# Performance work log

Hardware: AMD Instinct MI355X
Metric: run time of the kernel (lower is better)

## Reference

```python
import jax, jax.numpy as jnp
import numpy as np

EPS = 1e-7
R = 3  # routing iterations


def conv(x, k, b, stride):
    y = jax.lax.conv_general_dilated(x, k, (stride, stride), 'VALID',
                                     dimension_numbers=('NHWC', 'HWIO', 'NHWC'))
    return y + b


def squash(s):
    n = jnp.linalg.norm(s, axis=-1, keepdims=True)
    return (n * n) / (1.0 + n * n) * s / (n + EPS)


def setup_inputs() -> dict:
    key = jax.random.key(0)
    ks = jax.random.split(key, 12)
    B = 256

    def g(k, shape, scale=0.05):
        return jax.random.normal(k, shape, dtype=jnp.float32) * scale

    return dict(
        x=jax.random.normal(ks[0], (B, 40, 40, 1), dtype=jnp.float32),
        y=jax.random.randint(ks[1], (B,), 0, 10),
        conv1_k=g(ks[2], (5, 5, 1, 64)),   conv1_b=jnp.zeros((64,), jnp.float32),
        conv2_k=g(ks[3], (9, 9, 64, 128)), conv2_b=jnp.zeros((128,), jnp.float32),
        conv3_k=g(ks[4], (9, 9, 128, 256)), conv3_b=jnp.zeros((256,), jnp.float32),
        prim_k=g(ks[5], (9, 9, 256, 256)), prim_b=jnp.zeros((256,), jnp.float32),
        w=g(ks[6], (1152, 10, 16, 8)),
        d1_w=g(ks[7], (160, 1024)),  d1_b=jnp.zeros((1024,), jnp.float32),
        d2_w=g(ks[8], (1024, 2048)), d2_b=jnp.zeros((2048,), jnp.float32),
        d3_w=g(ks[9], (2048, 1600)), d3_b=jnp.zeros((1600,), jnp.float32),
    )


def reference(x, y, conv1_k, conv1_b, conv2_k, conv2_b, conv3_k, conv3_b,
              prim_k, prim_b, w, d1_w, d1_b, d2_w, d2_b, d3_w, d3_b):
    # conv stack: 40 -> 36 -> 28 -> 20 -> 6 (primary caps, stride 2, linear)
    h = jax.nn.relu(conv(x, conv1_k, conv1_b, 1))
    h = jax.nn.relu(conv(h, conv2_k, conv2_b, 1))
    h = jax.nn.relu(conv(h, conv3_k, conv3_b, 1))
    h = conv(h, prim_k, prim_b, 2)                      # [B,6,6,256]
    B = h.shape[0]
    u = h.reshape(B, 1152, 8)                           # 1152 primary capsules of dim 8

    # pose predictions: u_hat[b,i,j,k] = sum_v w[i,j,k,v] * u[b,i,v]
    u_hat = jnp.einsum('ijkv,biv->bijk', w, u)          # [B,1152,10,16]

    # dynamic routing by agreement
    b_logit = jnp.zeros((B, 1152, 10), dtype=u_hat.dtype)
    for _ in range(R):
        c = jax.nn.softmax(b_logit, axis=2)[..., None]          # [B,1152,10,1]
        s = jnp.sum(c * u_hat, axis=1, keepdims=True)           # [B,1,10,16]
        v = squash(s)                                           # [B,1,10,16]
        b_logit = b_logit + jnp.sum(u_hat * v, axis=-1)         # agreement

    # masking by true label and reconstruction
    yh = jax.nn.one_hot(y, 10, dtype=v.dtype)                   # [B,10]
    v_masked = yh[:, None, :, None] * v                         # [B,1,10,16]
    v_flat = v_masked.reshape(B, 10 * 16)
    r1 = jax.nn.relu(v_flat @ d1_w + d1_b)
    r2 = jax.nn.relu(r1 @ d2_w + d2_b)
    recon = jax.nn.sigmoid(r2 @ d3_w + d3_b)                    # [B,1600]
    return (v, recon)
```

## Files before the change

kernel.cpp:

```cpp
#include <hip/hip_runtime.h>
#include <hip/hip_bf16.h>

typedef _Float16 f16;
typedef __attribute__((ext_vector_type(8))) _Float16 f16x8;
typedef __attribute__((ext_vector_type(4))) float f32x4;

__device__ __forceinline__ void gload_lds16(const void* g, void* l) {
  __builtin_amdgcn_global_load_lds((const __attribute__((address_space(1))) void*)g,
                                   (__attribute__((address_space(3))) void*)l, 16, 0, 0);
}

__device__ __forceinline__ void wtrans_body(const float* __restrict__ src,
                                            f16* __restrict__ dst,
                                            int K, int N, int k0, int n0) {
  __shared__ float tile[64][65];
  int t = threadIdx.x;
#pragma unroll
  for (int i = 0; i < 16; ++i) {
    int id = t + i * 256;
    int r = id >> 6, c = id & 63;
    tile[r][c] = (n0 + c < N) ? src[(size_t)(k0 + r) * N + n0 + c] : 0.f;
  }
  __syncthreads();
#pragma unroll
  for (int i = 0; i < 16; ++i) {
    int id = t + i * 256;
    int r = id >> 6, c = id & 63;
    dst[(size_t)(n0 + r) * K + k0 + c] = (f16)tile[c][r];
  }
}

__global__ __launch_bounds__(256) void wprepc_kernel(const float* __restrict__ s0, f16* __restrict__ d0,
                                                     const float* __restrict__ s1, f16* __restrict__ d1,
                                                     const float* __restrict__ s2, f16* __restrict__ d2,
                                                     const float* __restrict__ x,
                                                     const float* __restrict__ c1k,
                                                     const float* __restrict__ c1b,
                                                     f16* __restrict__ h1) {
  int bid = (int)blockIdx.x;
  if (bid < 162) {
    int bx = bid % 81, by = bid / 81;
    wtrans_body(s0, d0, 5184, 128, bx * 64, by * 64);
  } else if (bid < 810) {
    int l = bid - 162; int bx = l % 162, by = l / 162;
    wtrans_body(s1, d1, 10368, 256, bx * 64, by * 64);
  } else if (bid < 2106) {
    int l = bid - 810; int bx = l % 324, by = l / 324;
    wtrans_body(s2, d2, 20736, 256, bx * 64, by * 64);
  } else {
    int idx = (bid - 2106) * 256 + threadIdx.x;
    int g = idx & 7;
    int co0 = g * 8;
    int r = idx >> 3;
    int ow = r % 36; int r2 = r / 36; int oh = r2 % 36; int b = r2 / 36;
    float acc[8];
#pragma unroll
    for (int j = 0; j < 8; ++j) acc[j] = c1b[co0 + j];
    const float* xp = x + (b * 40 + oh) * 40 + ow;
#pragma unroll
    for (int dy = 0; dy < 5; ++dy)
#pragma unroll
      for (int dx = 0; dx < 5; ++dx) {
        float xv = xp[dy * 40 + dx];
        const float* kp = c1k + (dy * 5 + dx) * 64 + co0;
#pragma unroll
        for (int j = 0; j < 8; ++j) acc[j] += xv * kp[j];
      }
    f16x8 o;
#pragma unroll
    for (int j = 0; j < 8; ++j) o[j] = (f16)fmaxf(acc[j], 0.f);
    *(f16x8*)(h1 + r * 64 + co0) = o;
  }
}

__global__ __launch_bounds__(256) void wprepd_kernel(const float* __restrict__ s0, f16* __restrict__ d0,
                                                     const float* __restrict__ s1, f16* __restrict__ d1) {
  int bid = (int)blockIdx.x;
  if (bid < 512) {
    int bx = bid % 16, by = bid / 16;
    wtrans_body(s0, d0, 1024, 2048, bx * 64, by * 64);
  } else {
    int l = bid - 512; int bx = l % 32, by = l / 32;
    wtrans_body(s1, d1, 2048, 1600, bx * 64, by * 64);
  }
}

template<int CIN, int WIN>
__device__ __forceinline__ int tapA_off(int kt) {
  int tap, ci0;
  if (CIN == 64)       { tap = kt;      ci0 = 0; }
  else if (CIN == 128) { tap = kt >> 1; ci0 = (kt & 1) << 6; }
  else                 { tap = kt >> 2; ci0 = (kt & 3) << 6; }
  int dy = tap / 9, dx = tap - dy * 9;
  return (dy * WIN + dx) * CIN + ci0;
}

template<int HIN, int WIN, int CIN, int HOUT, int WOUT, int COUT, int STRIDE,
         bool RELU, bool OUTF16, int FULLB, int TAILB>
__global__ __launch_bounds__(512, 2) void conv8p_kernel(const f16* __restrict__ in,
                                                        const f16* __restrict__ wt,
                                                        const float* __restrict__ bias,
                                                        f16* __restrict__ out16,
                                                        float* __restrict__ out32,
                                                        f16* __restrict__ tp01,
                                                        f16* __restrict__ tp2) {
  static_assert(COUT == 256, "BN=256 template requires COUT==256");
  constexpr int KTOT = 81 * CIN;
  constexpr int NT = KTOT / 64;
  static_assert(TAILB == 0 || NT % 3 == 0, "K-third split requires NT%3==0");
  constexpr int PNT = (TAILB > 0) ? NT / 3 : NT;
  __shared__ __align__(16) f16 lds[65536];
  const int bid = (int)blockIdx.x;
  int mb, kt0, kt1;
  f16* tp = nullptr;
  if (TAILB == 0 || bid < FULLB) {
    mb = bid; kt0 = 0; kt1 = NT;
  } else {
    int idx = bid - FULLB;
    int piece = idx / TAILB;
    int loc = idx - piece * TAILB;
    mb = FULLB + loc;
    kt0 = piece * PNT; kt1 = kt0 + PNT;
    tp = (piece < 2 ? tp01 + (size_t)piece * TAILB * 65536 : tp2) + (size_t)loc * 65536;
  }
  const int t = threadIdx.x;
  const int wave = t >> 6, lane = t & 63;
  const int hi = lane >> 4, lo = lane & 15;
  const int wm = wave >> 2, wn = wave & 3;

  int Aoff[4], Boff[4];
  {
    int g = (lane & 7) ^ ((lane >> 3) & 7);
#pragma unroll
    for (int rbi = 0; rbi < 4; ++rbi) {
      int r = rbi * 64 + 8 * wave + (lane >> 3);
      int m = mb * 256 + r;
      int b = m / (HOUT * WOUT);
      int rr = m - b * (HOUT * WOUT);
      int oh = rr / WOUT, ow = rr - oh * WOUT;
      Aoff[rbi] = ((b * HIN + oh * STRIDE) * WIN + ow * STRIDE) * CIN + g * 8;
      Boff[rbi] = r * KTOT + g * 8;
    }
  }
  const int gb0 = (hi ^ (lo & 7)) << 4;
  const int gb1 = ((4 + hi) ^ (lo & 7)) << 4;

  const char* ldsc = (const char*)lds;
  char* ldsw = (char*)lds;

#define GA(rbi, tpo, bq) gload_lds16(in + Aoff[rbi] + (tpo),                        \
    (void*)(ldsw + (bq) * 32768 + ((rbi) * 64 + 8 * wave) * 128))
#define GB(rbi, tile) gload_lds16(wt + Boff[rbi] + ((tile) << 6),                   \
    (void*)(ldsw + 65536 + ((tile) & 1) * 32768 + ((rbi) * 64 + 8 * wave) * 128))

  {
    int tq = tapA_off<CIN, WIN>(kt0);
    int bq = kt0 & 1;
    GA(0, tq, bq); GA(2, tq, bq); GA(1, tq, bq); GA(3, tq, bq);
    GB(0, kt0); GB(1, kt0); GB(2, kt0); GB(3, kt0);
    GB(0, kt0 + 1); GB(1, kt0 + 1); GB(2, kt0 + 1); GB(3, kt0 + 1);
    asm volatile("s_waitcnt vmcnt(4)" ::: "memory");
    __builtin_amdgcn_s_barrier();
  }

  f32x4 acc[8][4] = {};

#define DO_PHASE(Q, STAGE)                                                          \
  {                                                                                 \
    f16x8 af[2][2];                                                                 \
    _Pragma("unroll")                                                               \
    for (int mf = 0; mf < 2; ++mf) {                                                \
      af[mf][0] = *(const f16x8*)(Ab + ((Q) * 2 + mf) * 2048 + gb0);                \
      af[mf][1] = *(const f16x8*)(Ab + ((Q) * 2 + mf) * 2048 + gb1);                \
    }                                                                               \
    STAGE;                                                                          \
    __builtin_amdgcn_s_barrier();                                                   \
    asm volatile("s_waitcnt lgkmcnt(0)" ::: "memory");                              \
    __builtin_amdgcn_sched_barrier(0);                                              \
    __builtin_amdgcn_s_setprio(1);                                                  \
    _Pragma("unroll")                                                               \
    for (int sb = 0; sb < 2; ++sb)                                                  \
      _Pragma("unroll")                                                             \
      for (int mf = 0; mf < 2; ++mf)                                                \
        _Pragma("unroll")                                                           \
        for (int nf = 0; nf < 4; ++nf)                                              \
          acc[(Q) * 2 + mf][nf] = __builtin_amdgcn_mfma_f32_16x16x32_f16(           \
              af[mf][sb], bfr[nf][sb], acc[(Q) * 2 + mf][nf], 0, 0, 0);             \
    __builtin_amdgcn_s_setprio(0);                                                  \
    __builtin_amdgcn_s_barrier();                                                   \
  }

  for (int T = kt0; T < kt1; ++T) {
    const int q = T & 1;
    const char* Ab = ldsc + q * 32768 + wm * 16384 + lo * 128;
    const char* Bb = ldsc + 65536 + q * 32768 + wn * 8192 + lo * 128;
    const int tpn = tapA_off<CIN, WIN>(T + 1);
    f16x8 bfr[4][2];
#pragma unroll
    for (int nf = 0; nf < 4; ++nf) {
      bfr[nf][0] = *(const f16x8*)(Bb + nf * 2048 + gb0);
      bfr[nf][1] = *(const f16x8*)(Bb + nf * 2048 + gb1);
    }
    DO_PHASE(0, if (T + 1 < kt1) { GA(0, tpn, (T + 1) & 1); GA(2, tpn, (T + 1) & 1); })
    DO_PHASE(1, if (T + 1 < kt1) { GA(1, tpn, (T + 1) & 1); GA(3, tpn, (T + 1) & 1); })
    DO_PHASE(2, if (T + 2 < kt1) { GB(0, T + 2); GB(1, T + 2); })
    DO_PHASE(3,
      if (T + 2 < kt1) {
        GB(2, T + 2); GB(3, T + 2);
        asm volatile("s_waitcnt vmcnt(4)" ::: "memory");
      } else {
        asm volatile("s_waitcnt vmcnt(0)" ::: "memory");
      })
  }
#undef DO_PHASE
#undef GA
#undef GB

  if (tp == nullptr) {
#pragma unroll
    for (int mfr = 0; mfr < 8; ++mfr) {
#pragma unroll
      for (int nf = 0; nf < 4; ++nf) {
        int m0 = mb * 256 + wm * 128 + mfr * 16 + hi * 4;
        int n = wn * 64 + nf * 16 + lo;
        float bval = bias[n];
#pragma unroll
        for (int r = 0; r < 4; ++r) {
          float v = acc[mfr][nf][r] + bval;
          if (RELU) v = fmaxf(v, 0.f);
          int o = (m0 + r) * COUT + n;
          if (OUTF16) out16[o] = (f16)v; else out32[o] = v;
        }
      }
    }
  } else {
#pragma unroll
    for (int mfr = 0; mfr < 8; ++mfr) {
#pragma unroll
      for (int nf = 0; nf < 4; ++nf) {
        int rowloc = wm * 128 + mfr * 16 + hi * 4;
        int n = wn * 64 + nf * 16 + lo;
#pragma unroll
        for (int r = 0; r < 4; ++r)
          tp[(rowloc + r) * 256 + n] = (f16)acc[mfr][nf][r];
      }
    }
  }
}

__global__ __launch_bounds__(256) void tailred3_kernel(const f16* __restrict__ tp01,
                                                       const f16* __restrict__ tp2,
                                                       const float* __restrict__ bias,
                                                       f16* __restrict__ h3) {
  int idx = blockIdx.x * 256 + threadIdx.x;
  int e0 = idx * 8;
  int n0 = e0 & 255;
  f16x8 a = *(const f16x8*)(tp01 + e0);
  f16x8 b = *(const f16x8*)(tp01 + 9437184 + e0);
  f16x8 c = *(const f16x8*)(tp2 + e0);
  f16x8 o;
#pragma unroll
  for (int j = 0; j < 8; ++j) {
    float v = (float)a[j] + (float)b[j] + (float)c[j] + bias[n0 + j];
    o[j] = (f16)fmaxf(v, 0.f);
  }
  *(f16x8*)(h3 + 16777216 + e0) = o;
}

template<int HIN, int WIN, int CIN, int HOUT, int WOUT, int COUT, int STRIDE,
         bool RELU, bool OUTF16, int SPLIT, bool ADDBIAS>
__global__ __launch_bounds__(256) void conv_mfma_kernel(const f16* __restrict__ in,
                                                        const f16* __restrict__ wt,
                                                        const float* __restrict__ bias,
                                                        f16* __restrict__ out16,
                                                        float* __restrict__ out32) {
  constexpr int KTOT = 81 * CIN;
  constexpr int NBLK = COUT / 128;
  constexpr int MTOT = 256 * HOUT * WOUT;
  constexpr int MBNB = (MTOT / 128) * NBLK;
  constexpr int NKT = (KTOT / 64) / SPLIT;
  __shared__ __align__(16) f16 lds[16384];
  int bidx = (int)blockIdx.x;
  int ks = 0;
  if (SPLIT > 1) { ks = bidx / MBNB; bidx -= ks * MBNB; }
  const int mb = bidx / NBLK;
  const int nb = bidx % NBLK;
  const int t = threadIdx.x;
  const int wave = t >> 6, lane = t & 63;
  const int hi = lane >> 4, lo = lane & 15;
  const bool isA = wave < 2;
  const int slot0 = wave << 9;

  int baseoff[8];
#pragma unroll
  for (int it = 0; it < 8; ++it) {
    int s = slot0 + it * 64 + lane;
    if (isA) {
      int row = s >> 3;
      int g = (s & 7) ^ (row & 7);
      int mg = mb * 128 + row;
      int b = mg / (HOUT * WOUT);
      int rr = mg - b * (HOUT * WOUT);
      int oh = rr / WOUT;
      int ow = rr - oh * WOUT;
      baseoff[it] = ((b * HIN + oh * STRIDE) * WIN + ow * STRIDE) * CIN + g * 8;
    } else {
      int sl = s - 1024;
      int row = sl >> 3;
      int g = (sl & 7) ^ (row & 7);
      baseoff[it] = (nb * 128 + row) * KTOT + g * 8;
    }
  }
  const f16* gsrc = isA ? in : wt;

  int aQ[4], bQ[4];
  const int wm = wave >> 1, wn = wave & 1;
#pragma unroll
  for (int f = 0; f < 4; ++f) {
    int arow = wm * 64 + f * 16 + lo;
    aQ[f] = (arow * 128) ^ ((arow & 7) << 4);
    int brow = wn * 64 + f * 16 + lo;
    bQ[f] = 16384 + ((brow * 128) ^ ((brow & 7) << 4));
  }

  f32x4 acc[4][4] = {};
  const char* ldsc = (const char*)lds;

  const int kt0 = ks * NKT;
  for (int kt = kt0; kt < kt0 + NKT; ++kt) {
    int tapoff;
    if (isA) tapoff = tapA_off<CIN, WIN>(kt);
    else     tapoff = kt << 6;
    __syncthreads();
#pragma unroll
    for (int it = 0; it < 8; ++it)
      gload_lds16(gsrc + baseoff[it] + tapoff,
                  (void*)((char*)lds + ((slot0 + it * 64) << 4)));
    __syncthreads();
#pragma unroll
    for (int sub = 0; sub < 2; ++sub) {
      const int gx = (sub * 4 + hi) << 4;
      f16x8 av[4], bv[4];
#pragma unroll
      for (int f = 0; f < 4; ++f) av[f] = *(const f16x8*)(ldsc + (aQ[f] ^ gx));
#pragma unroll
      for (int f = 0; f < 4; ++f) bv[f] = *(const f16x8*)(ldsc + (bQ[f] ^ gx));
#pragma unroll
      for (int mf = 0; mf < 4; ++mf)
#pragma unroll
        for (int nf = 0; nf < 4; ++nf)
          acc[mf][nf] = __builtin_amdgcn_mfma_f32_16x16x32_f16(av[mf], bv[nf],
                                                               acc[mf][nf], 0, 0, 0);
    }
  }

  float* o32 = out32 + (size_t)ks * MTOT * COUT;
#pragma unroll
  for (int mf = 0; mf < 4; ++mf) {
#pragma unroll
    for (int nf = 0; nf < 4; ++nf) {
      int m0 = mb * 128 + wm * 64 + mf * 16 + hi * 4;
      int n = nb * 128 + wn * 64 + nf * 16 + lo;
      float bval = ADDBIAS ? bias[n] : 0.f;
#pragma unroll
      for (int r = 0; r < 4; ++r) {
        float v = acc[mf][nf][r] + bval;
        if (RELU) v = fmaxf(v, 0.f);
        int o = (m0 + r) * COUT + n;
        if (OUTF16) out16[o] = (f16)v; else o32[o] = v;
      }
    }
  }
}

template<int K, int NP, int SPLIT>
__global__ __launch_bounds__(256) void gemm_mfma_kernel(const f16* __restrict__ A,
                                                        const f16* __restrict__ Bw,
                                                        float* __restrict__ dpart) {
  constexpr int NBLK = NP / 128;
  constexpr int MBNB = 2 * NBLK;
  constexpr int NKT = (K / 64) / SPLIT;
  __shared__ __align__(16) f16 lds[16384];
  int bidx = (int)blockIdx.x;
  int ks = 0;
  if (SPLIT > 1) { ks = bidx / MBNB; bidx -= ks * MBNB; }
  const int mb = bidx / NBLK;
  const int nb = bidx % NBLK;
  const int t = threadIdx.x;
  const int wave = t >> 6, lane = t & 63;
  const int hi = lane >> 4, lo = lane & 15;
  const bool isA = wave < 2;
  const int slot0 = wave << 9;

  int baseoff[8];
#pragma unroll
  for (int it = 0; it < 8; ++it) {
    int s = slot0 + it * 64 + lane;
    if (isA) {
      int row = s >> 3;
      int g = (s & 7) ^ (row & 7);
      baseoff[it] = (mb * 128 + row) * K + g * 8;
    } else {
      int sl = s - 1024;
      int row = sl >> 3;
      int g = (sl & 7) ^ (row & 7);
      baseoff[it] = (nb * 128 + row) * K + g * 8;
    }
  }
  const f16* gsrc = isA ? A : Bw;

  int aQ[4], bQ[4];
  const int wm = wave >> 1, wn = wave & 1;
#pragma unroll
  for (int f = 0; f < 4; ++f) {
    int arow = wm * 64 + f * 16 + lo;
    aQ[f] = (arow * 128) ^ ((arow & 7) << 4);
    int brow = wn * 64 + f * 16 + lo;
    bQ[f] = 16384 + ((brow * 128) ^ ((brow & 7) << 4));
  }

  f32x4 acc[4][4] = {};
  const char* ldsc = (const char*)lds;

  const int kt0 = ks * NKT;
  for (int kt = kt0; kt < kt0 + NKT; ++kt) {
    int tapoff = kt << 6;
    __syncthreads();
#pragma unroll
    for (int it = 0; it < 8; ++it)
      gload_lds16(gsrc + baseoff[it] + tapoff,
                  (void*)((char*)lds + ((slot0 + it * 64) << 4)));
    __syncthreads();
#pragma unroll
    for (int sub = 0; sub < 2; ++sub) {
      const int gx = (sub * 4 + hi) << 4;
      f16x8 av[4], bv[4];
#pragma unroll
      for (int f = 0; f < 4; ++f) av[f] = *(const f16x8*)(ldsc + (aQ[f] ^ gx));
#pragma unroll
      for (int f = 0; f < 4; ++f) bv[f] = *(const f16x8*)(ldsc + (bQ[f] ^ gx));
#pragma unroll
      for (int mf = 0; mf < 4; ++mf)
#pragma unroll
        for (int nf = 0; nf < 4; ++nf)
          acc[mf][nf] = __builtin_amdgcn_mfma_f32_16x16x32_f16(av[mf], bv[nf],
                                                               acc[mf][nf], 0, 0, 0);
    }
  }

  float* o32 = dpart + (size_t)ks * 256 * NP;
#pragma unroll
  for (int mf = 0; mf < 4; ++mf) {
#pragma unroll
    for (int nf = 0; nf < 4; ++nf) {
      int m0 = mb * 128 + wm * 64 + mf * 16 + hi * 4;
      int n = nb * 128 + wn * 64 + nf * 16 + lo;
#pragma unroll
      for (int r = 0; r < 4; ++r)
        o32[(m0 + r) * NP + n] = acc[mf][nf][r];
    }
  }
}

__global__ __launch_bounds__(256) void d2red_kernel(const float* __restrict__ part,
                                                    const float* __restrict__ bias,
                                                    f16* __restrict__ r2) {
  int idx = blockIdx.x * 256 + threadIdx.x;
  int e0 = idx * 4;
  int n0 = e0 & 2047;
  float4 a = *(const float4*)(part + e0);
  const float4 b1 = *(const float4*)(part + 524288 + e0);
  const float4 b2 = *(const float4*)(part + 1048576 + e0);
  const float4 b3 = *(const float4*)(part + 1572864 + e0);
  float v[4] = {a.x + b1.x + b2.x + b3.x, a.y + b1.y + b2.y + b3.y,
                a.z + b1.z + b2.z + b3.z, a.w + b1.w + b2.w + b3.w};
#pragma unroll
  for (int j = 0; j < 4; ++j)
    r2[e0 + j] = (f16)fmaxf(v[j] + bias[n0 + j], 0.f);
}

__global__ __launch_bounds__(256) void d3red_kernel(const float* __restrict__ part,
                                                    const float* __restrict__ bias,
                                                    float* __restrict__ recon) {
  int idx = blockIdx.x * 256 + threadIdx.x;
  int e0 = idx * 4;
  int n0 = e0 % 1664;
  int m = e0 / 1664;
  float v[4] = {0.f, 0.f, 0.f, 0.f};
#pragma unroll
  for (int s = 0; s < 8; ++s) {
    float4 a = *(const float4*)(part + s * 425984 + e0);
    v[0] += a.x; v[1] += a.y; v[2] += a.z; v[3] += a.w;
  }
#pragma unroll
  for (int j = 0; j < 4; ++j) {
    int n = n0 + j;
    if (n < 1600)
      recon[m * 1600 + n] = 1.f / (1.f + expf(-(v[j] + bias[n])));
  }
}

__global__ __launch_bounds__(320) void uhatps_kernel(const float* __restrict__ wf,
                                                     const float* __restrict__ part,
                                                     const float* __restrict__ pbias,
                                                     f16* __restrict__ uh,
                                                     float* __restrict__ parts) {
  __shared__ float pl[8][128][8];
  int blk = (int)blockIdx.x;
  int ic = blk / 32, bg = blk - ic * 32;
  int b0 = bg * 8;
  int t = threadIdx.x;
  for (int e = t; e < 8192; e += 320) {
    int b8 = e >> 10;
    int el = e & 1023;
    float a = pbias[el & 255];
    int gi = (b0 + b8) * 9216 + ic * 1024 + el;
#pragma unroll
    for (int s = 0; s < 6; ++s) a += part[s * 2359296 + gi];
    pl[b8][el >> 3][el & 7] = a;
  }
  __syncthreads();
  int half = (t >= 160) ? 1 : 0;
  int jk = t - half * 160;
  int ibase = ic * 128 + half * 64;
  float sum[8] = {};
  for (int il = 0; il < 64; ++il) {
    int i = ibase + il;
    const float4* w4 = (const float4*)(wf + (i * 160 + jk) * 8);
    float4 w0 = w4[0], w1 = w4[1];
    int row = half * 64 + il;
#pragma unroll
    for (int b8 = 0; b8 < 8; ++b8) {
      const float* pr = pl[b8][row];
      float acc = w0.x * pr[0] + w0.y * pr[1] + w0.z * pr[2] + w0.w * pr[3] +
                  w1.x * pr[4] + w1.y * pr[5] + w1.z * pr[6] + w1.w * pr[7];
      uh[((size_t)(b0 + b8) * 1152 + i) * 160 + jk] = (f16)acc;
      sum[b8] += acc;
    }
  }
#pragma unroll
  for (int b8 = 0; b8 < 8; ++b8)
    parts[((b0 + b8) * 18 + ic * 2 + half) * 160 + jk] = sum[b8];
}

template<int NCH, bool FIRST, bool WRITEB>
__global__ __launch_bounds__(256) void ba_kernel(const f16* __restrict__ uh,
                                                 const float* __restrict__ psrc,
                                                 float cscale,
                                                 float* __restrict__ blog,
                                                 float* __restrict__ pdst) {
  __shared__ f16 ul[128 * 172];
  __shared__ float vl[160];
  __shared__ float csm[128 * 10];
  int blk = (int)blockIdx.x;
  int b = blk / 9, ic = blk - b * 9;
  int t = threadIdx.x;
  const f16* ub = uh + (size_t)(b * 1152 + ic * 128) * 160;
  for (int e = t; e < 2560; e += 256) {
    int row = e / 20, col = e - row * 20;
    *(f16x8*)(ul + row * 172 + col * 8) = *(const f16x8*)(ub + row * 160 + col * 8);
  }
  if (t < 160) {
    float s = 0.f;
    for (int c = 0; c < NCH; ++c) s += psrc[(b * NCH + c) * 160 + t];
    s *= cscale;
    float ss = s * s;
    ss += __shfl_xor(ss, 1, 16);
    ss += __shfl_xor(ss, 2, 16);
    ss += __shfl_xor(ss, 4, 16);
    ss += __shfl_xor(ss, 8, 16);
    float n = sqrtf(ss);
    float f = ss / ((1.f + ss) * (n + 1e-7f));
    vl[t] = f * s;
  }
  __syncthreads();

  int il = t >> 1, half = t & 1, j0 = half * 5;
  const f16* ur = ul + il * 172 + j0 * 16;
  float agr[5];
#pragma unroll
  for (int j = 0; j < 5; ++j) {
    f16x8 a0 = *(const f16x8*)(ur + j * 16);
    f16x8 a1 = *(const f16x8*)(ur + j * 16 + 8);
    const float* vv = vl + (j0 + j) * 16;
    float s = (float)a0[0] * vv[0] + (float)a0[1] * vv[1] + (float)a0[2] * vv[2] +
              (float)a0[3] * vv[3] + (float)a0[4] * vv[4] + (float)a0[5] * vv[5] +
              (float)a0[6] * vv[6] + (float)a0[7] * vv[7] +
              (float)a1[0] * vv[8] + (float)a1[1] * vv[9] + (float)a1[2] * vv[10] +
              (float)a1[3] * vv[11] + (float)a1[4] * vv[12] + (float)a1[5] * vv[13] +
              (float)a1[6] * vv[14] + (float)a1[7] * vv[15];
    agr[j] = s;
  }
  int bbase = (b * 1152 + ic * 128 + il) * 10 + j0;
  float bl[5];
#pragma unroll
  for (int j = 0; j < 5; ++j) bl[j] = (FIRST ? 0.f : blog[bbase + j]) + agr[j];
  if (WRITEB) {
#pragma unroll
    for (int j = 0; j < 5; ++j) blog[bbase + j] = bl[j];
  }
  float mx = bl[0];
#pragma unroll
  for (int j = 1; j < 5; ++j) mx = fmaxf(mx, bl[j]);
  mx = fmaxf(mx, __shfl_xor(mx, 1));
  float e5[5], se = 0.f;
#pragma unroll
  for (int j = 0; j < 5; ++j) { e5[j] = expf(bl[j] - mx); se += e5[j]; }
  se += __shfl_xor(se, 1);
  float inv = 1.f / se;
#pragma unroll
  for (int j = 0; j < 5; ++j) csm[il * 10 + j0 + j] = e5[j] * inv;
  __syncthreads();

  if (t < 160) {
    int j = t >> 4;
    float s = 0.f;
    for (int il2 = 0; il2 < 128; ++il2)
      s += csm[il2 * 10 + j] * (float)ul[il2 * 172 + t];
    pdst[(b * 9 + ic) * 160 + t] = s;
  }
}

__global__ __launch_bounds__(1024) void maskd1v_kernel(const float* __restrict__ parts,
                                                       const int* __restrict__ y,
                                                       const float* __restrict__ w1,
                                                       const float* __restrict__ b1,
                                                       float* __restrict__ vout,
                                                       f16* __restrict__ r1) {
  __shared__ float vl[160];
  int b = blockIdx.x, t = threadIdx.x;
  if (t < 160) {
    float s = 0.f;
    for (int c = 0; c < 9; ++c) s += parts[(b * 9 + c) * 160 + t];
    float ss = s * s;
    ss += __shfl_xor(ss, 1, 16);
    ss += __shfl_xor(ss, 2, 16);
    ss += __shfl_xor(ss, 4, 16);
    ss += __shfl_xor(ss, 8, 16);
    float n = sqrtf(ss);
    float f = ss / ((1.f + ss) * (n + 1e-7f));
    float v = f * s;
    vl[t] = v;
    vout[b * 160 + t] = v;
  }
  __syncthreads();
  int yb = y[b];
  float acc = b1[t];
#pragma unroll
  for (int k = 0; k < 16; ++k) acc += vl[yb * 16 + k] * w1[(yb * 16 + k) * 1024 + t];
  r1[b * 1024 + t] = (f16)fmaxf(acc, 0.f);
}

extern "C" void kernel_launch(void* const* d_in, const int* in_sizes, int n_in,
                              void* d_out, int out_size, void* d_ws, size_t ws_size,
                              hipStream_t stream) {
  const float* x       = (const float*)d_in[0];
  const int*   y       = (const int*)d_in[1];
  const float* conv1_k = (const float*)d_in[2];
  const float* conv1_b = (const float*)d_in[3];
  const float* conv2_k = (const float*)d_in[4];
  const float* conv2_b = (const float*)d_in[5];
  const float* conv3_k = (const float*)d_in[6];
  const float* conv3_b = (const float*)d_in[7];
  const float* prim_k  = (const float*)d_in[8];
  const float* prim_b  = (const float*)d_in[9];
  const float* w_route = (const float*)d_in[10];
  const float* d1_w = (const float*)d_in[11];
  const float* d1_b = (const float*)d_in[12];
  const float* d2_w = (const float*)d_in[13];
  const float* d2_b = (const float*)d_in[14];
  const float* d3_w = (const float*)d_in[15];
  const float* d3_b = (const float*)d_in[16];

  char* ws = (char*)d_ws;
  f16*   h1      = (f16*)(ws + 0);
  f16*   tpart01 = (f16*)(ws + 0);
  float* part    = (float*)(ws + 0);
  float* dpart2  = (float*)(ws + 0);
  float* dpart3  = (float*)(ws + 16777216);
  f16*   h2      = (f16*)(ws + 42467328);
  f16*   uhat    = (f16*)(ws + 56623104);
  f16*   h3      = (f16*)(ws + 93847552);
  f16*   tpart2  = (f16*)(ws + 146276352);
  float* parts_a = (float*)(ws + 150994944);
  float* parts_b = (float*)(ws + 153944064);
  float* blog    = (float*)(ws + 155713536);
  f16*   r1h     = (f16*)(ws + 167673856);
  f16*   r2h     = (f16*)(ws + 168198144);
  f16*   wt2     = (f16*)(ws + 170819584);
  f16*   wt3     = (f16*)(ws + 172146688);
  f16*   wtp     = (f16*)(ws + 177455104);
  f16*   wd2     = (f16*)(ws + 177455104);
  f16*   wd3     = (f16*)(ws + 181649408);

  float* vout  = (float*)d_out;
  float* recon = (float*)d_out + 40960;

  wprepc_kernel<<<12474, 256, 0, stream>>>(conv2_k, wt2, conv3_k, wt3, prim_k, wtp,
                                           x, conv1_k, conv1_b, h1);

  conv_mfma_kernel<36, 36, 64, 28, 28, 128, 1, true, true, 1, true>
      <<<1568, 256, 0, stream>>>(h1, wt2, conv2_b, h2, nullptr);
  conv8p_kernel<28, 28, 128, 20, 20, 256, 1, true, true, 256, 144>
      <<<688, 512, 0, stream>>>(h2, wt3, conv3_b, h3, nullptr, tpart01, tpart2);
  tailred3_kernel<<<4608, 256, 0, stream>>>(tpart01, tpart2, conv3_b, h3);
  conv_mfma_kernel<20, 20, 256, 6, 6, 256, 2, false, false, 6, false>
      <<<864, 256, 0, stream>>>(h3, wtp, prim_b, nullptr, part);

  uhatps_kernel<<<288, 320, 0, stream>>>(w_route, part, prim_b, uhat, parts_a);
  wprepd_kernel<<<1344, 256, 0, stream>>>(d2_w, wd2, d3_w, wd3);
  ba_kernel<18, true, true><<<2304, 256, 0, stream>>>(uhat, parts_a, 0.1f, blog, parts_b);
  ba_kernel<9, false, false><<<2304, 256, 0, stream>>>(uhat, parts_b, 1.0f, blog, parts_a);

  maskd1v_kernel<<<256, 1024, 0, stream>>>(parts_a, y, d1_w, d1_b, vout, r1h);
  gemm_mfma_kernel<1024, 2048, 4><<<128, 256, 0, stream>>>(r1h, wd2, dpart2);
  d2red_kernel<<<512, 256, 0, stream>>>(dpart2, d2_b, r2h);
  gemm_mfma_kernel<2048, 1664, 8><<<208, 256, 0, stream>>>(r2h, wd3, dpart3);
  d3red_kernel<<<416, 256, 0, stream>>>(dpart3, d3_b, recon);
}
```

Baseline: 1.147 ms.

## Port conv2 to 512-thread BN=128 MFMA kernel with K-split tail blocks

Replaces the conv2 implicit-GEMM kernel with a new 512-thread kernel that uses 512-row M tiles, 32-wide K steps, double-buffered direct-to-LDS loads and setprio-scheduled MFMA phases. It also splits the tail M blocks into three K-thirds so the grid balances across CUs. The partial sums from those blocks are written to scratch and combined by a new reduction kernel that adds bias and applies ReLU. The aim is better data reuse and load balance for conv2, at the cost of an extra kernel launch and scratch traffic for the tail partials.

```diff
diff --git a/kernel.cpp b/kernel.cpp
--- a/kernel.cpp
+++ b/kernel.cpp
@@ -91,6 +91,14 @@
   if (CIN == 64)       { tap = kt;      ci0 = 0; }
   else if (CIN == 128) { tap = kt >> 1; ci0 = (kt & 1) << 6; }
   else                 { tap = kt >> 2; ci0 = (kt & 3) << 6; }
+  int dy = tap / 9, dx = tap - dy * 9;
+  return (dy * WIN + dx) * CIN + ci0;
+}
+
+template<int CIN, int WIN>
+__device__ __forceinline__ int tap32_off(int kt) {
+  constexpr int CPT = CIN / 32;
+  int tap = kt / CPT, ci0 = (kt % CPT) * 32;
   int dy = tap / 9, dx = tap - dy * 9;
   return (dy * WIN + dx) * CIN + ci0;
 }
@@ -248,6 +256,180 @@
   }
 }
 
+template<int HIN, int WIN, int CIN, int HOUT, int WOUT, int COUT, int STRIDE,
+         bool RELU, int FULLB, int TAILB>
+__global__ __launch_bounds__(512, 2) void conv8pw_kernel(const f16* __restrict__ in,
+                                                         const f16* __restrict__ wt,
+                                                         const float* __restrict__ bias,
+                                                         f16* __restrict__ out16,
+                                                         f16* __restrict__ tp01,
+                                                         f16* __restrict__ tp2) {
+  static_assert(COUT == 128, "BN=128 template requires COUT==128");
+  constexpr int KTOT = 81 * CIN;
+  constexpr int NT = KTOT / 32;
+  static_assert(TAILB == 0 || NT % 3 == 0, "K-third split requires NT%3==0");
+  constexpr int PNT = (TAILB > 0) ? NT / 3 : NT;
+  __shared__ __align__(16) f16 lds[40960];
+  const int bid = (int)blockIdx.x;
+  int mb, kt0, kt1;
+  f16* tp = nullptr;
+  if (TAILB == 0 || bid < FULLB) {
+    mb = bid; kt0 = 0; kt1 = NT;
+  } else {
+    int idx = bid - FULLB;
+    int piece = idx / TAILB;
+    int loc = idx - piece * TAILB;
+    mb = FULLB + loc;
+    kt0 = piece * PNT; kt1 = kt0 + PNT;
+    tp = (piece < 2 ? tp01 + (size_t)piece * TAILB * 65536 : tp2) + (size_t)loc * 65536;
+  }
+  const int t = threadIdx.x;
+  const int wave = t >> 6, lane = t & 63;
+  const int hi = lane >> 4, lo = lane & 15;
+  const int wm = wave >> 1, wn = wave & 1;
+
+  int Aoff[4], Boff;
+  {
+    int g = (lane & 3) ^ ((lane >> 3) & 3);
+#pragma unroll
+    for (int c = 0; c < 4; ++c) {
+      int r = c * 128 + 16 * wave + (lane >> 2);
+      int m = mb * 512 + r;
+      int b = m / (HOUT * WOUT);
+      int rr = m - b * (HOUT * WOUT);
+      int oh = rr / WOUT, ow = rr - oh * WOUT;
+      Aoff[c] = ((b * HIN + oh * STRIDE) * WIN + ow * STRIDE) * CIN + g * 8;
+    }
+    Boff = (16 * wave + (lane >> 2)) * KTOT + g * 8;
+  }
+  const int gbx = (hi ^ ((lo >> 1) & 3)) << 4;
+
+  const char* ldsc = (const char*)lds;
+  char* ldsw = (char*)lds;
+
+#define GA(c, tpo, bq) gload_lds16(in + Aoff[c] + (tpo),                            \
+    (void*)(ldsw + (bq) * 32768 + ((c) * 128 + 16 * wave) * 64))
+#define GB(tile) gload_lds16(wt + Boff + (tile) * 32,                               \
+    (void*)(ldsw + 65536 + ((tile) & 1) * 8192 + (16 * wave) * 64))
+
+  {
+    int tq = tap32_off<CIN, WIN>(kt0);
+    int bq = kt0 & 1;
+    GA(0, tq, bq); GA(1, tq, bq); GA(2, tq, bq); GA(3, tq, bq);
+    GB(kt0); GB(kt0 + 1);
+    asm volatile("s_waitcnt vmcnt(1)" ::: "memory");
+    __builtin_amdgcn_s_barrier();
+  }
+
+  f32x4 acc[8][4] = {};
+
+  for (int T = kt0; T < kt1; ++T) {
+    const int q = T & 1;
+    const char* Ab = ldsc + q * 32768 + (wm * 128 + lo) * 64;
+    const char* Bb = ldsc + 65536 + q * 8192 + (wn * 64 + lo) * 64;
+    const int tpn = tap32_off<CIN, WIN>(T + 1);
+    f16x8 bfr[4];
+#pragma unroll
+    for (int nf = 0; nf < 4; ++nf)
+      bfr[nf] = *(const f16x8*)(Bb + nf * 1024 + gbx);
+    {
+      f16x8 af[4];
+#pragma unroll
+      for (int mf = 0; mf < 4; ++mf)
+        af[mf] = *(const f16x8*)(Ab + mf * 1024 + gbx);
+      if (T + 1 < kt1) { GA(0, tpn, (T + 1) & 1); GA(1, tpn, (T + 1) & 1); }
+      __builtin_amdgcn_s_barrier();
+      asm volatile("s_waitcnt lgkmcnt(0)" ::: "memory");
+      __builtin_amdgcn_sched_barrier(0);
+      __builtin_amdgcn_s_setprio(1);
+#pragma unroll
+      for (int mf = 0; mf < 4; ++mf)
+#pragma unroll
+        for (int nf = 0; nf < 4; ++nf)
+          acc[mf][nf] = __builtin_amdgcn_mfma_f32_16x16x32_f16(af[mf], bfr[nf],
+                                                               acc[mf][nf], 0, 0, 0);
+      __builtin_amdgcn_s_setprio(0);
+      __builtin_amdgcn_s_barrier();
+    }
+    {
+      f16x8 af[4];
+#pragma unroll
+      for (int mf = 0; mf < 4; ++mf)
+        af[mf] = *(const f16x8*)(Ab + (4 + mf) * 1024 + gbx);
+      if (T + 1 < kt1) { GA(2, tpn, (T + 1) & 1); GA(3, tpn, (T + 1) & 1); }
+      if (T + 2 < kt1) {
+        GB(T + 2);
+        asm volatile("s_waitcnt vmcnt(1)" ::: "memory");
+      } else {
+        asm volatile("s_waitcnt vmcnt(0)" ::: "memory");
+      }
+      __builtin_amdgcn_s_barrier();
+      asm volatile("s_waitcnt lgkmcnt(0)" ::: "memory");
+      __builtin_amdgcn_sched_barrier(0);
+      __builtin_amdgcn_s_setprio(1);
+#pragma unroll
+      for (int mf = 0; mf < 4; ++mf)
+#pragma unroll
+        for (int nf = 0; nf < 4; ++nf)
+          acc[4 + mf][nf] = __builtin_amdgcn_mfma_f32_16x16x32_f16(af[mf], bfr[nf],
+                                                                   acc[4 + mf][nf], 0, 0, 0);
+      __builtin_amdgcn_s_setprio(0);
+      __builtin_amdgcn_s_barrier();
+    }
+  }
+#undef GA
+#undef GB
+
+  if (tp == nullptr) {
+#pragma unroll
+    for (int mfr = 0; mfr < 8; ++mfr) {
+#pragma unroll
+      for (int nf = 0; nf < 4; ++nf) {
+        int m0 = mb * 512 + wm * 128 + mfr * 16 + hi * 4;
+        int n = wn * 64 + nf * 16 + lo;
+        float bval = bias[n];
+#pragma unroll
+        for (int r = 0; r < 4; ++r) {
+          float v = acc[mfr][nf][r] + bval;
+          if (RELU) v = fmaxf(v, 0.f);
+          out16[(m0 + r) * COUT + n] = (f16)v;
+        }
+      }
+    }
+  } else {
+#pragma unroll
+    for (int mfr = 0; mfr < 8; ++mfr) {
+#pragma unroll
+      for (int nf = 0; nf < 4; ++nf) {
+        int rowloc = wm * 128 + mfr * 16 + hi * 4;
+        int n = wn * 64 + nf * 16 + lo;
+#pragma unroll
+        for (int r = 0; r < 4; ++r)
+          tp[(rowloc + r) * 128 + n] = (f16)acc[mfr][nf][r];
+      }
+    }
+  }
+}
+
+__global__ __launch_bounds__(256) void tailredw_kernel(const f16* __restrict__ tp01,
+                                                       const f16* __restrict__ tp2,
+                                                       const float* __restrict__ bias,
+                                                       f16* __restrict__ h2) {
+  int idx = blockIdx.x * 256 + threadIdx.x;
+  int e0 = idx * 8;
+  int n0 = e0 & 127;
+  f16x8 a = *(const f16x8*)(tp01 + e0);
+  f16x8 b = *(const f16x8*)(tp01 + 8912896 + e0);
+  f16x8 c = *(const f16x8*)(tp2 + e0);
+  f16x8 o;
+#pragma unroll
+  for (int j = 0; j < 8; ++j) {
+    float v = (float)a[j] + (float)b[j] + (float)c[j] + bias[n0 + j];
+    o[j] = (f16)fmaxf(v, 0.f);
+  }
+  *(f16x8*)(h2 + 16777216 + e0) = o;
+}
+
 __global__ __launch_bounds__(256) void tailred3_kernel(const f16* __restrict__ tp01,
                                                        const f16* __restrict__ tp2,
                                                        const float* __restrict__ bias,
@@ -681,6 +863,8 @@
   f16*   h2      = (f16*)(ws + 42467328);
   f16*   uhat    = (f16*)(ws + 56623104);
   f16*   h3      = (f16*)(ws + 93847552);
+  f16*   tpc2_01 = (f16*)(ws + 93847552);
+  f16*   tpc2_2  = (f16*)(ws + 129499136);
   f16*   tpart2  = (f16*)(ws + 146276352);
   float* parts_a = (float*)(ws + 150994944);
   float* parts_b = (float*)(ws + 153944064);
@@ -699,8 +883,9 @@
   wprepc_kernel<<<12474, 256, 0, stream>>>(conv2_k, wt2, conv3_k, wt3, prim_k, wtp,
                                            x, conv1_k, conv1_b, h1);
 
-  conv_mfma_kernel<36, 36, 64, 28, 28, 128, 1, true, true, 1, true>
-      <<<1568, 256, 0, stream>>>(h1, wt2, conv2_b, h2, nullptr);
+  conv8pw_kernel<36, 36, 64, 28, 28, 128, 1, true, 256, 136>
+      <<<664, 512, 0, stream>>>(h1, wt2, conv2_b, h2, tpc2_01, tpc2_2);
+  tailredw_kernel<<<4352, 256, 0, stream>>>(tpc2_01, tpc2_2, conv2_b, h2);
   conv8p_kernel<28, 28, 128, 20, 20, 256, 1, true, true, 256, 144>
       <<<688, 512, 0, stream>>>(h2, wt3, conv3_b, h3, nullptr, tpart01, tpart2);
   tailred3_kernel<<<4608, 256, 0, stream>>>(tpart01, tpart2, conv3_b, h3);
```

Measured after the change: 1.119 ms. 2.5% less time.
